# Kernel optimization log

Hardware: AMD Instinct MI355X
Metric: run time of the kernel (lower is better)

## Reference

```python
import jax, jax.numpy as jnp
import numpy as np

B, CIN, H, W = 16, 1, 256, 256
WIDTH = 64
MODES = 32
LAYERS = 4
COUT = 1


def conv1x1(x, w, b):
    # x: [B,Ci,H,W], w: [Co,Ci], b: [Co]
    return jnp.einsum('bixy,oi->boxy', x, w) + b[None, :, None, None]


def mlp(x, w1, b1, w2, b2):
    # Conv2d(ci,mid,1) -> GELU(exact) -> Conv2d(mid,co,1)
    return conv1x1(jax.nn.gelu(conv1x1(x, w1, b1), approximate=False), w2, b2)


def spectral_conv2d(x, w1r, w1i, w2r, w2i):
    # x: [B,C,H,W]; weights: [Ci,Co,m1,m2] (real/imag parts of cfloat params)
    b, c, h, w = x.shape
    m1, m2 = w1r.shape[2], w1r.shape[3]
    co = w1r.shape[1]
    x_ft = jnp.fft.rfft2(x)  # [B,C,H,W//2+1] complex64
    w1 = w1r + 1j * w1i
    w2 = w2r + 1j * w2i
    top = jnp.einsum('bixy,ioxy->boxy', x_ft[:, :, :m1, :m2], w1)
    bot = jnp.einsum('bixy,ioxy->boxy', x_ft[:, :, -m1:, :m2], w2)
    out_ft = jnp.zeros((b, co, h, w // 2 + 1), dtype=x_ft.dtype)
    out_ft = out_ft.at[:, :, :m1, :m2].set(top).at[:, :, -m1:, :m2].set(bot)
    return jnp.fft.irfft2(out_ft, s=(h, w))


def setup_inputs() -> dict:
    key = jax.random.key(0)
    ks = iter(jax.random.split(key, 32))
    scale = 1.0 / (WIDTH * WIDTH)
    f32 = jnp.float32
    inp = {}
    inp['x'] = jax.random.normal(next(ks), (B, CIN, H, W), dtype=f32)
    # lifting 1x1 conv
    inp['p_w'] = jax.random.normal(next(ks), (WIDTH, CIN), dtype=f32) / np.sqrt(CIN)
    inp['p_b'] = jnp.zeros((WIDTH,), dtype=f32)
    # per-layer spectral weights (real/imag of uniform cfloat init)
    shp = (LAYERS, WIDTH, WIDTH, MODES, MODES)
    inp['sw1r'] = scale * jax.random.uniform(next(ks), shp, dtype=f32)
    inp['sw1i'] = scale * jax.random.uniform(next(ks), shp, dtype=f32)
    inp['sw2r'] = scale * jax.random.uniform(next(ks), shp, dtype=f32)
    inp['sw2i'] = scale * jax.random.uniform(next(ks), shp, dtype=f32)
    # per-layer channel MLP (mid_channels = WIDTH)
    inp['m1w'] = jax.random.normal(next(ks), (LAYERS, WIDTH, WIDTH), dtype=f32) / np.sqrt(WIDTH)
    inp['m1b'] = jnp.zeros((LAYERS, WIDTH), dtype=f32)
    inp['m2w'] = jax.random.normal(next(ks), (LAYERS, WIDTH, WIDTH), dtype=f32) / np.sqrt(WIDTH)
    inp['m2b'] = jnp.zeros((LAYERS, WIDTH), dtype=f32)
    # per-layer skip 1x1 conv
    inp['skw'] = jax.random.normal(next(ks), (LAYERS, WIDTH, WIDTH), dtype=f32) / np.sqrt(WIDTH)
    inp['skb'] = jnp.zeros((LAYERS, WIDTH), dtype=f32)
    # projection MLP (mid = 4*WIDTH)
    inp['q1w'] = jax.random.normal(next(ks), (4 * WIDTH, WIDTH), dtype=f32) / np.sqrt(WIDTH)
    inp['q1b'] = jnp.zeros((4 * WIDTH,), dtype=f32)
    inp['q2w'] = jax.random.normal(next(ks), (COUT, 4 * WIDTH), dtype=f32) / np.sqrt(4 * WIDTH)
    inp['q2b'] = jnp.zeros((COUT,), dtype=f32)
    return inp


def reference(x, p_w, p_b, sw1r, sw1i, sw2r, sw2i, m1w, m1b, m2w, m2b,
              skw, skb, q1w, q1b, q2w, q2b):
    h = conv1x1(x, p_w, p_b)  # lift to [B,WIDTH,H,W]
    for l in range(LAYERS):
        x1 = spectral_conv2d(h, sw1r[l], sw1i[l], sw2r[l], sw2i[l])
        x1 = mlp(x1, m1w[l], m1b[l], m2w[l], m2b[l])
        x2 = conv1x1(h, skw[l], skb[l])
        h = x1 + x2
        if l < LAYERS - 1:
            h = jax.nn.gelu(h, approximate=False)
    return mlp(h, q1w, q1b, q2w, q2b)  # [B,COUT,H,W]
```

## Files before the change

kernel.cpp:

```cpp
#include <hip/hip_runtime.h>
#include <math.h>

#define NC 64
#define NH 256
#define NW 256
#define NM 32
#define NKY 64
#define HW 65536

typedef short bfrag __attribute__((ext_vector_type(8)));
typedef float facc  __attribute__((ext_vector_type(4)));
#define MFMA(a,b,c) __builtin_amdgcn_mfma_f32_16x16x32_bf16(a,b,c,0,0,0)

static constexpr float PI_F = 3.14159265358979323846f;

__device__ __forceinline__ unsigned short f2b(float f) {
  unsigned b = __float_as_uint(f);
  return (unsigned short)((b + 0x7FFFu + ((b >> 16) & 1u)) >> 16);
}
__device__ __forceinline__ float b2f(unsigned short h) {
  return __uint_as_float((unsigned)h << 16);
}
__device__ __forceinline__ unsigned packsplit(float v) {
  unsigned short hi = f2b(v);
  unsigned short lo = f2b(v - b2f(hi));
  return (unsigned)hi | ((unsigned)lo << 16);
}

__device__ __forceinline__ float gelu_f(float x) {
  float z = fabsf(x) * 0.70710678118654752f;
  float t = 1.0f / (1.0f + 0.3275911f * z);
  float e = __expf(-z * z);
  float p = t * (0.254829592f + t * (-0.284496736f + t * (1.421413741f +
            t * (-1.453152027f + t * 1.061405429f))));
  float er = copysignf(1.0f - p * e, x);
  return 0.5f * x * (1.0f + er);
}

__global__ void k_tEy(unsigned short* __restrict__ eh, unsigned short* __restrict__ el) {
  int i = blockIdx.x * 256 + threadIdx.x;
  int m = i >> 8, y = i & 255;
  int kyi = m & 63;
  int ky = (kyi < 32) ? kyi : (192 + kyi);
  int a = (ky * y) & 255;
  float s, c; sincosf((float)a * (PI_F / 128.f), &s, &c);
  float v = (m < 64) ? c : -s;
  unsigned short h = f2b(v);
  eh[i] = h; el[i] = f2b(v - b2f(h));
}
__global__ void k_tEx(unsigned short* __restrict__ eh, unsigned short* __restrict__ el) {
  int i = blockIdx.x * 256 + threadIdx.x;
  int m = i >> 9, k = i & 511;
  int x = k & 255, plane = k >> 8, kx = m & 31;
  int a = (kx * x) & 255;
  float s, c; sincosf((float)a * (PI_F / 128.f), &s, &c);
  float v = (m < 32) ? (plane ? s : c) : (plane ? c : -s);
  unsigned short h = f2b(v);
  eh[i] = h; el[i] = f2b(v - b2f(h));
}
__global__ void k_tWy(unsigned short* __restrict__ eh, unsigned short* __restrict__ el) {
  int i = blockIdx.x * 256 + threadIdx.x;
  int row = i >> 7, k = i & 127;
  int y = row & 255, part = row >> 8;
  int kyi = k & 63, plane = k >> 6;
  int ky = (kyi < 32) ? kyi : (192 + kyi);
  int a = (ky * y) & 255;
  float s, c; sincosf((float)a * (PI_F / 128.f), &s, &c);
  float v = (part == 0) ? (plane ? -s : c) : (plane ? c : s);
  unsigned short h = f2b(v);
  eh[i] = h; el[i] = f2b(v - b2f(h));
}
__global__ void k_tCx(unsigned short* __restrict__ eh, unsigned short* __restrict__ el) {
  int i = blockIdx.x * 256 + threadIdx.x;
  int x = i >> 6, k = i & 63;
  int kx = k & 31, plane = k >> 5;
  float w = ((kx == 0) ? 1.0f : 2.0f) / 65536.0f;
  int a = (kx * x) & 255;
  float s, c; sincosf((float)a * (PI_F / 128.f), &s, &c);
  float v = plane ? (-w * s) : (w * c);
  unsigned short h = f2b(v);
  eh[i] = h; el[i] = f2b(v - b2f(h));
}

__global__ void k_cvt2(const float* __restrict__ src, unsigned short* __restrict__ hi,
                       unsigned short* __restrict__ lo, int n) {
  int i = blockIdx.x * 256 + threadIdx.x;
  if (i < n) {
    float v = src[i];
    unsigned short h = f2b(v);
    hi[i] = h;
    lo[i] = f2b(v - b2f(h));
  }
}

__global__ __launch_bounds__(256) void k_lift(const float* __restrict__ x,
                                              const float* __restrict__ pw,
                                              const float* __restrict__ pb,
                                              unsigned* __restrict__ hp) {
  int b = blockIdx.y;
  int yx = blockIdx.x * 256 + threadIdx.x;
  float v = x[(size_t)b * HW + yx];
  size_t o = (size_t)b * NC * HW + yx;
  for (int c = 0; c < NC; ++c)
    hp[o + (size_t)c * HW] = packsplit(v * pw[c] + pb[c]);
}

__global__ __launch_bounds__(256) void k_fy2(const unsigned* __restrict__ hp,
                                             const unsigned short* __restrict__ Ah,
                                             const unsigned short* __restrict__ Al,
                                             float* __restrict__ Xc, int Ncol) {
  int tid = threadIdx.x, wv = tid >> 6, ln = tid & 63, g16 = ln >> 4, l15 = ln & 15;
  int colbase = blockIdx.x * 128 + wv * 32;
  int rowb = blockIdx.y * 64;
  facc acc[4][2];
#pragma unroll
  for (int mf = 0; mf < 4; ++mf)
#pragma unroll
    for (int pf = 0; pf < 2; ++pf) acc[mf][pf] = (facc)0.f;
#pragma unroll 1
  for (int ks = 0; ks < 8; ++ks) {
    int kof = g16 * 8 + 32 * ks;
    bfrag bh[2], bl[2];
#pragma unroll
    for (int pf = 0; pf < 2; ++pf) {
      int col = colbase + pf * 16 + l15;
      size_t o = (size_t)(col >> 8) * HW + (col & 255) + (size_t)kof * 256;
#pragma unroll
      for (int j = 0; j < 8; ++j) {
        unsigned u = hp[o + j * 256];
        bh[pf][j] = (short)(u & 0xffffu);
        bl[pf][j] = (short)(u >> 16);
      }
    }
#pragma unroll
    for (int mf = 0; mf < 4; ++mf) {
      int row = rowb + 16 * mf + l15;
      bfrag ah = *(const bfrag*)(Ah + row * 256 + kof);
      bfrag al = *(const bfrag*)(Al + row * 256 + kof);
#pragma unroll
      for (int pf = 0; pf < 2; ++pf) {
        acc[mf][pf] = MFMA(ah, bh[pf], acc[mf][pf]);
        acc[mf][pf] = MFMA(ah, bl[pf], acc[mf][pf]);
        acc[mf][pf] = MFMA(al, bh[pf], acc[mf][pf]);
      }
    }
  }
#pragma unroll
  for (int mf = 0; mf < 4; ++mf)
#pragma unroll
    for (int pf = 0; pf < 2; ++pf) {
      int col = colbase + pf * 16 + l15;
#pragma unroll
      for (int r = 0; r < 4; ++r)
        Xc[(size_t)(rowb + 16 * mf + 4 * g16 + r) * Ncol + col] = acc[mf][pf][r];
    }
}

__global__ __launch_bounds__(256) void k_fx2(const float* __restrict__ Xc,
                                             const unsigned short* __restrict__ Ah,
                                             const unsigned short* __restrict__ Al,
                                             float* __restrict__ X2r,
                                             float* __restrict__ X2i, int NcXc) {
  int tid = threadIdx.x, wv = tid >> 6, ln = tid & 63, g16 = ln >> 4, l15 = ln & 15;
  int colbase = blockIdx.x * 64 + wv * 16;
  int mb = blockIdx.y * 2;
  facc acc[2];
  acc[0] = (facc)0.f; acc[1] = (facc)0.f;
#pragma unroll 1
  for (int ks = 0; ks < 16; ++ks) {
    int plane = ks >> 3;
    int x0 = (ks & 7) * 32 + g16 * 8;
    int kof = g16 * 8 + 32 * ks;
    bfrag bh, bl;
    {
      int col = colbase + l15;
      const float* p = Xc + (size_t)(plane * 64 + (col & 63)) * NcXc + (col >> 6) * 256 + x0;
      float4 u0 = *(const float4*)p;
      float4 u1 = *(const float4*)(p + 4);
      float tv[8] = {u0.x, u0.y, u0.z, u0.w, u1.x, u1.y, u1.z, u1.w};
#pragma unroll
      for (int j = 0; j < 8; ++j) {
        unsigned short hi = f2b(tv[j]);
        bh[j] = (short)hi;
        bl[j] = (short)f2b(tv[j] - b2f(hi));
      }
    }
#pragma unroll
    for (int mf = 0; mf < 2; ++mf) {
      int row = (mb + mf) * 16 + l15;
      bfrag ah = *(const bfrag*)(Ah + row * 512 + kof);
      bfrag al = *(const bfrag*)(Al + row * 512 + kof);
      acc[mf] = MFMA(ah, bh, acc[mf]);
      acc[mf] = MFMA(ah, bl, acc[mf]);
      acc[mf] = MFMA(al, bh, acc[mf]);
    }
  }
#pragma unroll
  for (int mf = 0; mf < 2; ++mf) {
    int col = colbase + l15;
    int mfg = mb + mf;
    float* base = (mfg >= 2) ? X2i : X2r;
    int kxb = 16 * (mfg & 1) + 4 * g16;
    float4 v = make_float4(acc[mf][0], acc[mf][1], acc[mf][2], acc[mf][3]);
    *(float4*)(base + (size_t)col * 32 + kxb) = v;
  }
}

__global__ __launch_bounds__(512) void k_spec(const float* __restrict__ X2r,
                                              const float* __restrict__ X2i,
                                              const float* __restrict__ w1r,
                                              const float* __restrict__ w1i,
                                              const float* __restrict__ w2r,
                                              const float* __restrict__ w2i,
                                              float* __restrict__ S, int Ncs) {
  int b = blockIdx.y;
  int och = blockIdx.x & 3;
  int kyi = blockIdx.x >> 2;
  __shared__ float2 xs[NC * NM];
  for (int idx = threadIdx.x; idx < NC * NM; idx += 512) {
    int i = idx >> 5, kx = idx & 31;
    size_t c2 = ((size_t)(b * 64 + i) * 64 + kyi) * 32 + kx;
    xs[idx] = make_float2(X2r[c2], X2i[c2]);
  }
  __syncthreads();
  int kx = threadIdx.x & 31;
  int ol = threadIdx.x >> 5;
  int o = och * 16 + ol;
  int kym = kyi & 31;
  const float* wr = (kyi < 32) ? w1r : w2r;
  const float* wi = (kyi < 32) ? w1i : w2i;
  size_t wb = ((size_t)o * NM + kym) * NM + kx;
  float ar = 0.f, ai = 0.f;
#pragma unroll 4
  for (int i = 0; i < NC; ++i) {
    float2 xv = xs[i * NM + kx];
    float wrv = wr[wb + (size_t)i * 65536];
    float wiv = wi[wb + (size_t)i * 65536];
    ar += xv.x * wrv - xv.y * wiv;
    ai += xv.x * wiv + xv.y * wrv;
  }
  size_t cco = (size_t)(b * 64 + o) * 32 + kx;
  S[(size_t)kyi * Ncs + cco] = ar;
  S[(size_t)(64 + kyi) * Ncs + cco] = ai;
}

__global__ __launch_bounds__(256) void k_iy2(const float* __restrict__ S,
                                             const unsigned short* __restrict__ Ah,
                                             const unsigned short* __restrict__ Al,
                                             float* __restrict__ t2, int Ncs) {
  int tid = threadIdx.x, wv = tid >> 6, ln = tid & 63, g16 = ln >> 4, l15 = ln & 15;
  int colbase = blockIdx.x * 128 + wv * 32;
  int rowb = blockIdx.y * 32;
  facc acc[2][2];
#pragma unroll
  for (int mf = 0; mf < 2; ++mf)
#pragma unroll
    for (int pf = 0; pf < 2; ++pf) acc[mf][pf] = (facc)0.f;
#pragma unroll 1
  for (int ks = 0; ks < 4; ++ks) {
    int kof = g16 * 8 + 32 * ks;
    bfrag bh[2], bl[2];
#pragma unroll
    for (int pf = 0; pf < 2; ++pf) {
      int col = colbase + pf * 16 + l15;
      const float* p = S + (size_t)kof * Ncs + col;
#pragma unroll
      for (int j = 0; j < 8; ++j) {
        float v = p[(size_t)j * Ncs];
        unsigned short hi = f2b(v);
        bh[pf][j] = (short)hi;
        bl[pf][j] = (short)f2b(v - b2f(hi));
      }
    }
#pragma unroll
    for (int mf = 0; mf < 2; ++mf) {
      int row = rowb + 16 * mf + l15;
      bfrag ah = *(const bfrag*)(Ah + row * 128 + kof);
      bfrag al = *(const bfrag*)(Al + row * 128 + kof);
#pragma unroll
      for (int pf = 0; pf < 2; ++pf) {
        acc[mf][pf] = MFMA(ah, bh[pf], acc[mf][pf]);
        acc[mf][pf] = MFMA(ah, bl[pf], acc[mf][pf]);
        acc[mf][pf] = MFMA(al, bh[pf], acc[mf][pf]);
      }
    }
  }
#pragma unroll
  for (int mf = 0; mf < 2; ++mf)
#pragma unroll
    for (int pf = 0; pf < 2; ++pf) {
      int col = colbase + pf * 16 + l15;
#pragma unroll
      for (int r = 0; r < 4; ++r)
        t2[(size_t)(rowb + 16 * mf + 4 * g16 + r) * Ncs + col] = acc[mf][pf][r];
    }
}

__global__ __launch_bounds__(256) void k_ix2(const float* __restrict__ t2,
                                             const unsigned short* __restrict__ Ah,
                                             const unsigned short* __restrict__ Al,
                                             unsigned* __restrict__ x1p, int Nct) {
  int tid = threadIdx.x, wv = tid >> 6, ln = tid & 63, g16 = ln >> 4, l15 = ln & 15;
  int colbase = blockIdx.x * 128 + wv * 32;
  int rowb = blockIdx.y * 64;
  facc acc[4][2];
#pragma unroll
  for (int mf = 0; mf < 4; ++mf)
#pragma unroll
    for (int pf = 0; pf < 2; ++pf) acc[mf][pf] = (facc)0.f;
#pragma unroll 1
  for (int ks = 0; ks < 2; ++ks) {
    int kof = g16 * 8 + 32 * ks;
    bfrag bh[2], bl[2];
#pragma unroll
    for (int pf = 0; pf < 2; ++pf) {
      int col = colbase + pf * 16 + l15;
      const float* p = t2 + (size_t)(ks * 256 + (col & 255)) * Nct + (col >> 8) * 32 + g16 * 8;
      float4 u0 = *(const float4*)p;
      float4 u1 = *(const float4*)(p + 4);
      float tv[8] = {u0.x, u0.y, u0.z, u0.w, u1.x, u1.y, u1.z, u1.w};
#pragma unroll
      for (int j = 0; j < 8; ++j) {
        unsigned short hi = f2b(tv[j]);
        bh[pf][j] = (short)hi;
        bl[pf][j] = (short)f2b(tv[j] - b2f(hi));
      }
    }
#pragma unroll
    for (int mf = 0; mf < 4; ++mf) {
      int row = rowb + 16 * mf + l15;
      bfrag ah = *(const bfrag*)(Ah + row * 64 + kof);
      bfrag al = *(const bfrag*)(Al + row * 64 + kof);
#pragma unroll
      for (int pf = 0; pf < 2; ++pf) {
        acc[mf][pf] = MFMA(ah, bh[pf], acc[mf][pf]);
        acc[mf][pf] = MFMA(ah, bl[pf], acc[mf][pf]);
        acc[mf][pf] = MFMA(al, bh[pf], acc[mf][pf]);
      }
    }
  }
#pragma unroll
  for (int mf = 0; mf < 4; ++mf)
#pragma unroll
    for (int pf = 0; pf < 2; ++pf) {
      int col = colbase + pf * 16 + l15;
      int bc = col >> 8, y = col & 255;
      int xb = rowb + 16 * mf + 4 * g16;
      uint4 pv;
      pv.x = packsplit(acc[mf][pf][0]);
      pv.y = packsplit(acc[mf][pf][1]);
      pv.z = packsplit(acc[mf][pf][2]);
      pv.w = packsplit(acc[mf][pf][3]);
      size_t o = (size_t)bc * HW + y * 256 + xb;
      *(uint4*)(x1p + o) = pv;
    }
}

__global__ __launch_bounds__(128) void k_fmlp(const unsigned* __restrict__ x1p,
                                              unsigned* __restrict__ Hp,
                                              const unsigned short* __restrict__ w1h,
                                              const unsigned short* __restrict__ w1l,
                                              const float* __restrict__ b1p,
                                              const unsigned short* __restrict__ w2h,
                                              const unsigned short* __restrict__ w2l,
                                              const unsigned short* __restrict__ skh,
                                              const unsigned short* __restrict__ skl,
                                              const float* __restrict__ b2p,
                                              const float* __restrict__ skbp,
                                              int do_gelu) {
  __shared__ float mids[2][32 * 33];
  int tid = threadIdx.x, wv = tid >> 6, ln = tid & 63, g16 = ln >> 4, l15 = ln & 15;
  int b = blockIdx.y;
  int pxb = blockIdx.x * 64 + wv * 32;
  const unsigned* xq = x1p + (size_t)b * NC * HW;
  unsigned* hb = Hp + (size_t)b * NC * HW;

  facc a1[4][2];
#pragma unroll
  for (int mf = 0; mf < 4; ++mf)
#pragma unroll
    for (int pf = 0; pf < 2; ++pf) {
      facc z;
#pragma unroll
      for (int r = 0; r < 4; ++r) z[r] = b1p[16 * mf + 4 * g16 + r];
      a1[mf][pf] = z;
    }
#pragma unroll
  for (int ks = 0; ks < 2; ++ks) {
    bfrag xhb[2], xlb[2];
#pragma unroll
    for (int pf = 0; pf < 2; ++pf) {
      int px = pxb + pf * 16 + l15;
#pragma unroll
      for (int j = 0; j < 8; ++j) {
        int c = g16 * 8 + j + 32 * ks;
        unsigned u = xq[(size_t)c * HW + px];
        xhb[pf][j] = (short)(u & 0xffffu);
        xlb[pf][j] = (short)(u >> 16);
      }
    }
#pragma unroll
    for (int mf = 0; mf < 4; ++mf) {
      bfrag ah = *(const bfrag*)(w1h + (16 * mf + l15) * 64 + g16 * 8 + 32 * ks);
      bfrag al = *(const bfrag*)(w1l + (16 * mf + l15) * 64 + g16 * 8 + 32 * ks);
#pragma unroll
      for (int pf = 0; pf < 2; ++pf) {
        a1[mf][pf] = MFMA(ah, xhb[pf], a1[mf][pf]);
        a1[mf][pf] = MFMA(ah, xlb[pf], a1[mf][pf]);
        a1[mf][pf] = MFMA(al, xhb[pf], a1[mf][pf]);
      }
    }
  }

  facc a2[4][2];
#pragma unroll
  for (int mf = 0; mf < 4; ++mf)
#pragma unroll
    for (int pf = 0; pf < 2; ++pf) {
      facc z;
#pragma unroll
      for (int r = 0; r < 4; ++r) {
        int o = 16 * mf + 4 * g16 + r;
        z[r] = b2p[o] + skbp[o];
      }
      a2[mf][pf] = z;
    }
  float* mw = mids[wv];
#pragma unroll
  for (int ks = 0; ks < 2; ++ks) {
#pragma unroll
    for (int mm = 0; mm < 2; ++mm) {
      int mfh = 2 * ks + mm;
#pragma unroll
      for (int pf = 0; pf < 2; ++pf)
#pragma unroll
        for (int r = 0; r < 4; ++r)
          mw[(16 * mm + 4 * g16 + r) * 33 + pf * 16 + l15] = gelu_f(a1[mfh][pf][r]);
    }
    bfrag mhb[2], mlb[2], hhb[2], hlb[2];
#pragma unroll
    for (int pf = 0; pf < 2; ++pf) {
      int px = pxb + pf * 16 + l15;
#pragma unroll
      for (int j = 0; j < 8; ++j) {
        int c = g16 * 8 + j + 32 * ks;
        float v = mw[(g16 * 8 + j) * 33 + pf * 16 + l15];
        unsigned short hi = f2b(v);
        mhb[pf][j] = (short)hi;
        mlb[pf][j] = (short)f2b(v - b2f(hi));
        unsigned u = hb[(size_t)c * HW + px];
        hhb[pf][j] = (short)(u & 0xffffu);
        hlb[pf][j] = (short)(u >> 16);
      }
    }
#pragma unroll
    for (int mf = 0; mf < 4; ++mf) {
      bfrag w2hf = *(const bfrag*)(w2h + (16 * mf + l15) * 64 + g16 * 8 + 32 * ks);
      bfrag w2lf = *(const bfrag*)(w2l + (16 * mf + l15) * 64 + g16 * 8 + 32 * ks);
      bfrag skhf = *(const bfrag*)(skh + (16 * mf + l15) * 64 + g16 * 8 + 32 * ks);
      bfrag sklf = *(const bfrag*)(skl + (16 * mf + l15) * 64 + g16 * 8 + 32 * ks);
#pragma unroll
      for (int pf = 0; pf < 2; ++pf) {
        a2[mf][pf] = MFMA(w2hf, mhb[pf], a2[mf][pf]);
        a2[mf][pf] = MFMA(w2hf, mlb[pf], a2[mf][pf]);
        a2[mf][pf] = MFMA(w2lf, mhb[pf], a2[mf][pf]);
        a2[mf][pf] = MFMA(skhf, hhb[pf], a2[mf][pf]);
        a2[mf][pf] = MFMA(skhf, hlb[pf], a2[mf][pf]);
        a2[mf][pf] = MFMA(sklf, hhb[pf], a2[mf][pf]);
      }
    }
  }
#pragma unroll
  for (int mf = 0; mf < 4; ++mf)
#pragma unroll
    for (int pf = 0; pf < 2; ++pf) {
      facc v = a2[mf][pf];
      if (do_gelu) {
        v[0] = gelu_f(v[0]); v[1] = gelu_f(v[1]);
        v[2] = gelu_f(v[2]); v[3] = gelu_f(v[3]);
      }
      int px = pxb + pf * 16 + l15;
#pragma unroll
      for (int r = 0; r < 4; ++r)
        hb[(size_t)(16 * mf + 4 * g16 + r) * HW + px] = packsplit(v[r]);
    }
}

__global__ __launch_bounds__(256) void k_pproj(const unsigned* __restrict__ hp,
                                               const unsigned short* __restrict__ q1h,
                                               const unsigned short* __restrict__ q1l,
                                               const float* __restrict__ q1bp,
                                               const float* __restrict__ q2wp,
                                               const float* __restrict__ q2bp,
                                               float* __restrict__ out,
                                               int R0, int accum) {
  __shared__ unsigned short q1sh[128 * 72];
  __shared__ unsigned short q1sl[128 * 72];
  __shared__ float q1bs[128], q2s[128];
  int tid = threadIdx.x;
  for (int i = tid; i < 2048; i += 256) {
    int row = i >> 4, c4 = (i & 15) * 4;
    ushort4 vh = *(const ushort4*)(q1h + (size_t)(R0 + row) * 64 + c4);
    ushort4 vl = *(const ushort4*)(q1l + (size_t)(R0 + row) * 64 + c4);
    *(ushort4*)(q1sh + row * 72 + c4) = vh;
    *(ushort4*)(q1sl + row * 72 + c4) = vl;
  }
  if (tid < 128) {
    q1bs[tid] = q1bp[R0 + tid];
    q2s[tid] = q2wp[R0 + tid];
  }
  int wv = tid >> 6, ln = tid & 63, g16 = ln >> 4, l15 = ln & 15;
  float q2bias = q2bp[0];
  __syncthreads();

  int colbase = blockIdx.x * 128 + wv * 32;
  facc acc[8][2];
#pragma unroll
  for (int mf = 0; mf < 8; ++mf)
#pragma unroll
    for (int pf = 0; pf < 2; ++pf) {
      facc z;
#pragma unroll
      for (int r = 0; r < 4; ++r) z[r] = q1bs[16 * mf + 4 * g16 + r];
      acc[mf][pf] = z;
    }
#pragma unroll
  for (int ks = 0; ks < 2; ++ks) {
    bfrag bh[2], bl[2];
#pragma unroll
    for (int pf = 0; pf < 2; ++pf) {
      int col = colbase + pf * 16 + l15;
      size_t o = (size_t)(col >> 16) * NC * HW + (col & 65535);
#pragma unroll
      for (int j = 0; j < 8; ++j) {
        int c = g16 * 8 + j + 32 * ks;
        unsigned u = hp[o + (size_t)c * HW];
        bh[pf][j] = (short)(u & 0xffffu);
        bl[pf][j] = (short)(u >> 16);
      }
    }
#pragma unroll
    for (int mf = 0; mf < 8; ++mf) {
      bfrag ah = *(const bfrag*)(q1sh + (16 * mf + l15) * 72 + g16 * 8 + 32 * ks);
      bfrag al = *(const bfrag*)(q1sl + (16 * mf + l15) * 72 + g16 * 8 + 32 * ks);
#pragma unroll
      for (int pf = 0; pf < 2; ++pf) {
        acc[mf][pf] = MFMA(ah, bh[pf], acc[mf][pf]);
        acc[mf][pf] = MFMA(ah, bl[pf], acc[mf][pf]);
        acc[mf][pf] = MFMA(al, bh[pf], acc[mf][pf]);
      }
    }
  }
#pragma unroll
  for (int pf = 0; pf < 2; ++pf) {
    float partial = 0.f;
#pragma unroll
    for (int mf = 0; mf < 8; ++mf)
#pragma unroll
      for (int r = 0; r < 4; ++r)
        partial += gelu_f(acc[mf][pf][r]) * q2s[16 * mf + 4 * g16 + r];
    partial += __shfl_xor(partial, 16);
    partial += __shfl_xor(partial, 32);
    if (ln < 16) {
      int col = colbase + pf * 16 + ln;
      if (accum) out[col] += partial;
      else out[col] = partial + q2bias;
    }
  }
}

extern "C" void kernel_launch(void* const* d_in, const int* in_sizes, int n_in,
                              void* d_out, int out_size, void* d_ws, size_t ws_size,
                              hipStream_t stream) {
  const float* x    = (const float*)d_in[0];
  const float* p_w  = (const float*)d_in[1];
  const float* p_b  = (const float*)d_in[2];
  const float* sw1r = (const float*)d_in[3];
  const float* sw1i = (const float*)d_in[4];
  const float* sw2r = (const float*)d_in[5];
  const float* sw2i = (const float*)d_in[6];
  const float* m1w  = (const float*)d_in[7];
  const float* m1b  = (const float*)d_in[8];
  const float* m2w  = (const float*)d_in[9];
  const float* m2b  = (const float*)d_in[10];
  const float* skw  = (const float*)d_in[11];
  const float* skb  = (const float*)d_in[12];
  const float* q1w  = (const float*)d_in[13];
  const float* q1b  = (const float*)d_in[14];
  const float* q2w  = (const float*)d_in[15];
  const float* q2b  = (const float*)d_in[16];

  const size_t MB = 1048576ULL;
  const size_t TBL = 1 * MB;
  int g = 16;
  while (g > 1 && (size_t)g * 36 * MB + TBL > ws_size) g >>= 1;
  if ((size_t)g * 36 * MB + TBL > ws_size) return;

  char* wsb = (char*)d_ws;
  unsigned short* Eyh = (unsigned short*)(wsb + 0);
  unsigned short* Eyl = (unsigned short*)(wsb + 65536);
  unsigned short* Exh = (unsigned short*)(wsb + 131072);
  unsigned short* Exl = (unsigned short*)(wsb + 196608);
  unsigned short* Wyh = (unsigned short*)(wsb + 262144);
  unsigned short* Wyl = (unsigned short*)(wsb + 393216);
  unsigned short* Cxh = (unsigned short*)(wsb + 524288);
  unsigned short* Cxl = (unsigned short*)(wsb + 557056);
  unsigned short* m1h = (unsigned short*)(wsb + 589824);
  unsigned short* m1l = (unsigned short*)(wsb + 622592);
  unsigned short* m2h = (unsigned short*)(wsb + 655360);
  unsigned short* m2l = (unsigned short*)(wsb + 688128);
  unsigned short* skh = (unsigned short*)(wsb + 720896);
  unsigned short* skl = (unsigned short*)(wsb + 753664);
  unsigned short* q1h = (unsigned short*)(wsb + 786432);
  unsigned short* q1l = (unsigned short*)(wsb + 819200);

  char* base = wsb + TBL;
  unsigned* Hp  = (unsigned*)base;
  unsigned* x1p = (unsigned*)(base + (size_t)g * 16 * MB);
  float* Xc  = (float*)x1p;
  float* X2r = (float*)(base + (size_t)g * 24 * MB);
  float* X2i = (float*)(base + (size_t)g * 24 * MB + (size_t)g * 524288ULL);
  float* S   = (float*)(base + (size_t)g * 25 * MB);
  float* t2  = (float*)(base + (size_t)g * 32 * MB);

  k_tEy<<<128, 256, 0, stream>>>(Eyh, Eyl);
  k_tEx<<<128, 256, 0, stream>>>(Exh, Exl);
  k_tWy<<<256, 256, 0, stream>>>(Wyh, Wyl);
  k_tCx<<<64, 256, 0, stream>>>(Cxh, Cxl);
  k_cvt2<<<64, 256, 0, stream>>>(m1w, m1h, m1l, 16384);
  k_cvt2<<<64, 256, 0, stream>>>(m2w, m2h, m2l, 16384);
  k_cvt2<<<64, 256, 0, stream>>>(skw, skh, skl, 16384);
  k_cvt2<<<64, 256, 0, stream>>>(q1w, q1h, q1l, 16384);

  int Nfy = g * 16384;
  int Ncs = g * 2048;

  for (int b0 = 0; b0 < 16; b0 += g) {
    k_lift<<<dim3(256, g), 256, 0, stream>>>(x + (size_t)b0 * HW, p_w, p_b, Hp);
    for (int l = 0; l < 4; ++l) {
      k_fy2<<<dim3(g * 128, 2), 256, 0, stream>>>(Hp, Eyh, Eyl, Xc, Nfy);
      k_fx2<<<dim3(g * 64, 2), 256, 0, stream>>>(Xc, Exh, Exl, X2r, X2i, Nfy);
      k_spec<<<dim3(256, g), 512, 0, stream>>>(X2r, X2i,
                                               sw1r + (size_t)l * 4194304,
                                               sw1i + (size_t)l * 4194304,
                                               sw2r + (size_t)l * 4194304,
                                               sw2i + (size_t)l * 4194304, S, Ncs);
      k_iy2<<<dim3(g * 16, 16), 256, 0, stream>>>(S, Wyh, Wyl, t2, Ncs);
      k_ix2<<<dim3(g * 128, 4), 256, 0, stream>>>(t2, Cxh, Cxl, x1p, Ncs);
      k_fmlp<<<dim3(1024, g), 128, 0, stream>>>(x1p, Hp,
                                                m1h + l * 4096, m1l + l * 4096, m1b + l * 64,
                                                m2h + l * 4096, m2l + l * 4096,
                                                skh + l * 4096, skl + l * 4096,
                                                m2b + l * 64, skb + l * 64, (l < 3) ? 1 : 0);
    }
    float* outc = (float*)d_out + (size_t)b0 * HW;
    k_pproj<<<g * 512, 256, 0, stream>>>(Hp, q1h, q1l, q1b, q2w, q2b, outc, 0, 0);
    k_pproj<<<g * 512, 256, 0, stream>>>(Hp, q1h, q1l, q1b, q2w, q2b, outc, 128, 1);
  }
}
```

Measured before the change: 3.812 ms.

## Stage fused MLP tiles in swizzled shared memory and split output channels across waves

```diff
diff --git a/kernel.cpp b/kernel.cpp
--- a/kernel.cpp
+++ b/kernel.cpp
@@ -25,6 +25,9 @@
   unsigned short hi = f2b(v);
   unsigned short lo = f2b(v - b2f(hi));
   return (unsigned)hi | ((unsigned)lo << 16);
+}
+__device__ __forceinline__ int swz(int ch, int px) {
+  return ch * 64 + (px ^ (((ch >> 3) & 3) << 4));
 }
 
 __device__ __forceinline__ float gelu_f(float x) {
@@ -356,7 +359,7 @@
     }
 }
 
-__global__ __launch_bounds__(128) void k_fmlp(const unsigned* __restrict__ x1p,
+__global__ __launch_bounds__(256) void k_fmlp(const unsigned* __restrict__ x1p,
                                               unsigned* __restrict__ Hp,
                                               const unsigned short* __restrict__ w1h,
                                               const unsigned short* __restrict__ w1l,
@@ -368,122 +371,115 @@
                                               const float* __restrict__ b2p,
                                               const float* __restrict__ skbp,
                                               int do_gelu) {
-  __shared__ float mids[2][32 * 33];
+  __shared__ unsigned xt[64 * 64];
+  __shared__ unsigned ht[64 * 64];
   int tid = threadIdx.x, wv = tid >> 6, ln = tid & 63, g16 = ln >> 4, l15 = ln & 15;
   int b = blockIdx.y;
-  int pxb = blockIdx.x * 64 + wv * 32;
+  int px0 = blockIdx.x * 64;
   const unsigned* xq = x1p + (size_t)b * NC * HW;
-  unsigned* hb = Hp + (size_t)b * NC * HW;
-
-  facc a1[4][2];
-#pragma unroll
-  for (int mf = 0; mf < 4; ++mf)
-#pragma unroll
-    for (int pf = 0; pf < 2; ++pf) {
-      facc z;
-#pragma unroll
-      for (int r = 0; r < 4; ++r) z[r] = b1p[16 * mf + 4 * g16 + r];
-      a1[mf][pf] = z;
-    }
+  unsigned* hq = Hp + (size_t)b * NC * HW;
+
+  for (int i = tid; i < 1024; i += 256) {
+    int ch = i >> 4, q = (i & 15) * 4;
+    int la = swz(ch, q);
+    *(uint4*)(xt + la) = *(const uint4*)(xq + (size_t)ch * HW + px0 + q);
+    *(uint4*)(ht + la) = *(const uint4*)(hq + (size_t)ch * HW + px0 + q);
+  }
+  __syncthreads();
+
+  int rw = 16 * wv;
+
+  facc a1[4];
+#pragma unroll
+  for (int pf = 0; pf < 4; ++pf) {
+    facc z;
+#pragma unroll
+    for (int r = 0; r < 4; ++r) z[r] = b1p[rw + 4 * g16 + r];
+    a1[pf] = z;
+  }
 #pragma unroll
   for (int ks = 0; ks < 2; ++ks) {
-    bfrag xhb[2], xlb[2];
-#pragma unroll
-    for (int pf = 0; pf < 2; ++pf) {
-      int px = pxb + pf * 16 + l15;
+    bfrag ah = *(const bfrag*)(w1h + (rw + l15) * 64 + g16 * 8 + 32 * ks);
+    bfrag al = *(const bfrag*)(w1l + (rw + l15) * 64 + g16 * 8 + 32 * ks);
+#pragma unroll
+    for (int pf = 0; pf < 4; ++pf) {
+      bfrag bh, bl;
 #pragma unroll
       for (int j = 0; j < 8; ++j) {
-        int c = g16 * 8 + j + 32 * ks;
-        unsigned u = xq[(size_t)c * HW + px];
-        xhb[pf][j] = (short)(u & 0xffffu);
-        xlb[pf][j] = (short)(u >> 16);
-      }
-    }
-#pragma unroll
-    for (int mf = 0; mf < 4; ++mf) {
-      bfrag ah = *(const bfrag*)(w1h + (16 * mf + l15) * 64 + g16 * 8 + 32 * ks);
-      bfrag al = *(const bfrag*)(w1l + (16 * mf + l15) * 64 + g16 * 8 + 32 * ks);
-#pragma unroll
-      for (int pf = 0; pf < 2; ++pf) {
-        a1[mf][pf] = MFMA(ah, xhb[pf], a1[mf][pf]);
-        a1[mf][pf] = MFMA(ah, xlb[pf], a1[mf][pf]);
-        a1[mf][pf] = MFMA(al, xhb[pf], a1[mf][pf]);
-      }
-    }
-  }
-
-  facc a2[4][2];
-#pragma unroll
-  for (int mf = 0; mf < 4; ++mf)
-#pragma unroll
-    for (int pf = 0; pf < 2; ++pf) {
-      facc z;
-#pragma unroll
-      for (int r = 0; r < 4; ++r) {
-        int o = 16 * mf + 4 * g16 + r;
-        z[r] = b2p[o] + skbp[o];
-      }
-      a2[mf][pf] = z;
-    }
-  float* mw = mids[wv];
+        int ch = g16 * 8 + j + 32 * ks;
+        unsigned u = xt[swz(ch, pf * 16 + l15)];
+        bh[j] = (short)(u & 0xffffu);
+        bl[j] = (short)(u >> 16);
+      }
+      a1[pf] = MFMA(ah, bh, a1[pf]);
+      a1[pf] = MFMA(ah, bl, a1[pf]);
+      a1[pf] = MFMA(al, bh, a1[pf]);
+    }
+  }
+  __syncthreads();
+
+#pragma unroll
+  for (int pf = 0; pf < 4; ++pf)
+#pragma unroll
+    for (int r = 0; r < 4; ++r)
+      xt[swz(rw + 4 * g16 + r, pf * 16 + l15)] = packsplit(gelu_f(a1[pf][r]));
+  __syncthreads();
+
+  facc a2[4];
+#pragma unroll
+  for (int pf = 0; pf < 4; ++pf) {
+    facc z;
+#pragma unroll
+    for (int r = 0; r < 4; ++r) {
+      int o = rw + 4 * g16 + r;
+      z[r] = b2p[o] + skbp[o];
+    }
+    a2[pf] = z;
+  }
 #pragma unroll
   for (int ks = 0; ks < 2; ++ks) {
-#pragma unroll
-    for (int mm = 0; mm < 2; ++mm) {
-      int mfh = 2 * ks + mm;
-#pragma unroll
-      for (int pf = 0; pf < 2; ++pf)
-#pragma unroll
-        for (int r = 0; r < 4; ++r)
-          mw[(16 * mm + 4 * g16 + r) * 33 + pf * 16 + l15] = gelu_f(a1[mfh][pf][r]);
-    }
-    bfrag mhb[2], mlb[2], hhb[2], hlb[2];
-#pragma unroll
-    for (int pf = 0; pf < 2; ++pf) {
-      int px = pxb + pf * 16 + l15;
+    bfrag w2hf = *(const bfrag*)(w2h + (rw + l15) * 64 + g16 * 8 + 32 * ks);
+    bfrag w2lf = *(const bfrag*)(w2l + (rw + l15) * 64 + g16 * 8 + 32 * ks);
+    bfrag skhf = *(const bfrag*)(skh + (rw + l15) * 64 + g16 * 8 + 32 * ks);
+    bfrag sklf = *(const bfrag*)(skl + (rw + l15) * 64 + g16 * 8 + 32 * ks);
+#pragma unroll
+    for (int pf = 0; pf < 4; ++pf) {
+      bfrag mhb, mlb, hhb, hlb;
 #pragma unroll
       for (int j = 0; j < 8; ++j) {
-        int c = g16 * 8 + j + 32 * ks;
-        float v = mw[(g16 * 8 + j) * 33 + pf * 16 + l15];
-        unsigned short hi = f2b(v);
-        mhb[pf][j] = (short)hi;
-        mlb[pf][j] = (short)f2b(v - b2f(hi));
-        unsigned u = hb[(size_t)c * HW + px];
-        hhb[pf][j] = (short)(u & 0xffffu);
-        hlb[pf][j] = (short)(u >> 16);
-      }
-    }
-#pragma unroll
-    for (int mf = 0; mf < 4; ++mf) {
-      bfrag w2hf = *(const bfrag*)(w2h + (16 * mf + l15) * 64 + g16 * 8 + 32 * ks);
-      bfrag w2lf = *(const bfrag*)(w2l + (16 * mf + l15) * 64 + g16 * 8 + 32 * ks);
-      bfrag skhf = *(const bfrag*)(skh + (16 * mf + l15) * 64 + g16 * 8 + 32 * ks);
-      bfrag sklf = *(const bfrag*)(skl + (16 * mf + l15) * 64 + g16 * 8 + 32 * ks);
-#pragma unroll
-      for (int pf = 0; pf < 2; ++pf) {
-        a2[mf][pf] = MFMA(w2hf, mhb[pf], a2[mf][pf]);
-        a2[mf][pf] = MFMA(w2hf, mlb[pf], a2[mf][pf]);
-        a2[mf][pf] = MFMA(w2lf, mhb[pf], a2[mf][pf]);
-        a2[mf][pf] = MFMA(skhf, hhb[pf], a2[mf][pf]);
-        a2[mf][pf] = MFMA(skhf, hlb[pf], a2[mf][pf]);
-        a2[mf][pf] = MFMA(sklf, hhb[pf], a2[mf][pf]);
-      }
-    }
-  }
-#pragma unroll
-  for (int mf = 0; mf < 4; ++mf)
-#pragma unroll
-    for (int pf = 0; pf < 2; ++pf) {
-      facc v = a2[mf][pf];
-      if (do_gelu) {
-        v[0] = gelu_f(v[0]); v[1] = gelu_f(v[1]);
-        v[2] = gelu_f(v[2]); v[3] = gelu_f(v[3]);
-      }
-      int px = pxb + pf * 16 + l15;
-#pragma unroll
-      for (int r = 0; r < 4; ++r)
-        hb[(size_t)(16 * mf + 4 * g16 + r) * HW + px] = packsplit(v[r]);
-    }
+        int ch = g16 * 8 + j + 32 * ks;
+        int la = swz(ch, pf * 16 + l15);
+        unsigned um = xt[la];
+        mhb[j] = (short)(um & 0xffffu);
+        mlb[j] = (short)(um >> 16);
+        unsigned uh = ht[la];
+        hhb[j] = (short)(uh & 0xffffu);
+        hlb[j] = (short)(uh >> 16);
+      }
+      a2[pf] = MFMA(w2hf, mhb, a2[pf]);
+      a2[pf] = MFMA(w2hf, mlb, a2[pf]);
+      a2[pf] = MFMA(w2lf, mhb, a2[pf]);
+      a2[pf] = MFMA(skhf, hhb, a2[pf]);
+      a2[pf] = MFMA(skhf, hlb, a2[pf]);
+      a2[pf] = MFMA(sklf, hhb, a2[pf]);
+    }
+  }
+  __syncthreads();
+
+#pragma unroll
+  for (int pf = 0; pf < 4; ++pf)
+#pragma unroll
+    for (int r = 0; r < 4; ++r) {
+      float v = a2[pf][r];
+      if (do_gelu) v = gelu_f(v);
+      ht[swz(rw + 4 * g16 + r, pf * 16 + l15)] = packsplit(v);
+    }
+  __syncthreads();
+
+  for (int i = tid; i < 1024; i += 256) {
+    int ch = i >> 4, q = (i & 15) * 4;
+    *(uint4*)(hq + (size_t)ch * HW + px0 + q) = *(const uint4*)(ht + swz(ch, q));
+  }
 }
 
 __global__ __launch_bounds__(256) void k_pproj(const unsigned* __restrict__ hp,
@@ -647,7 +643,7 @@
                                                sw2i + (size_t)l * 4194304, S, Ncs);
       k_iy2<<<dim3(g * 16, 16), 256, 0, stream>>>(S, Wyh, Wyl, t2, Ncs);
       k_ix2<<<dim3(g * 128, 4), 256, 0, stream>>>(t2, Cxh, Cxl, x1p, Ncs);
-      k_fmlp<<<dim3(1024, g), 128, 0, stream>>>(x1p, Hp,
+      k_fmlp<<<dim3(1024, g), 256, 0, stream>>>(x1p, Hp,
                                                 m1h + l * 4096, m1l + l * 4096, m1b + l * 64,
                                                 m2h + l * 4096, m2l + l * 4096,
                                                 skh + l * 4096, skl + l * 4096,
```

New measurement: 3.533 ms. 1.08x faster.
